# Performance work log

Hardware: AMD Instinct MI355X
Metric: run time of the kernel (lower is better)

The kernel has to match this reference:

```python
import jax, jax.numpy as jnp
import numpy as np


def setup_inputs() -> dict:
    key = jax.random.key(0)
    ks = jax.random.split(key, 6)
    dim, dt_rank, dim_inner, d_state, channels, batch = 1024, 64, 1024, 128, 64, 8
    rn = lambda k, shape, sc: (jax.random.normal(k, shape, jnp.float32) * sc)
    return {
        "x": rn(ks[0], (batch, channels, dim), 1.0),
        "proj_w": rn(ks[1], (dim, dim), dim ** -0.5),
        "proj_b": jnp.zeros((dim,), jnp.float32),
        "conv_w": rn(ks[2], (channels, channels, 3), (channels * 3) ** -0.5),
        "conv_b": jnp.zeros((channels,), jnp.float32),
        "deltaBC_w": rn(ks[3], (dt_rank + 2 * d_state, dim), dim ** -0.5),
        "dt_proj_w": rn(ks[4], (dim_inner, dt_rank), dt_rank ** -0.5),
        "dt_proj_b": jnp.zeros((dim_inner,), jnp.float32),
        "A_log": jnp.log(jnp.broadcast_to(
            jnp.arange(1, d_state + 1, dtype=jnp.float32), (dim_inner, d_state))),
        "D": jnp.ones((dim_inner,), jnp.float32),
    }


def _silu(x):
    return x * jax.nn.sigmoid(x)


def _selective_scan(x, delta, A, B, C, D):
    # x, delta: (b, l, ed); A: (ed, n); B, C: (b, l, n); D: (ed)
    deltaA = jnp.exp(delta[..., None] * A)                      # (b, l, ed, n)
    BX = delta[..., None] * B[:, :, None, :] * x[..., None]     # (b, l, ed, n)

    def binop(e1, e2):
        a1, b1 = e1
        a2, b2 = e2
        return a1 * a2, a2 * b1 + b2

    # h_t = deltaA_t * h_{t-1} + BX_t  (parallel scan over sequence axis)
    _, hs = jax.lax.associative_scan(binop, (deltaA, BX), axis=1)
    y = jnp.einsum("blen,bln->ble", hs, C) + D * x
    return y


def reference(x, proj_w, proj_b, conv_w, conv_b, deltaBC_w,
              dt_proj_w, dt_proj_b, A_log, D):
    dt_rank = dt_proj_w.shape[1]
    d_state = A_log.shape[1]

    skip = x
    # same self.proj applied to both branches
    x1 = x @ proj_w.T + proj_b
    x2 = x1

    # Conv1d over the feature axis, treating seq positions as channels (L == channels)
    x1 = jax.lax.conv_general_dilated(
        x1, conv_w, window_strides=(1,), padding=[(1, 1)],
        dimension_numbers=("NCH", "OIH", "NCH")) + conv_b[None, :, None]
    x1 = _silu(x1)

    # SSM
    A = -jnp.exp(A_log)
    dbc = x1 @ deltaBC_w.T                                      # (b, l, dt_rank + 2n)
    delta = dbc[..., :dt_rank]
    Bm = dbc[..., dt_rank:dt_rank + d_state]
    Cm = dbc[..., dt_rank + d_state:]
    delta = jax.nn.softplus(delta @ dt_proj_w.T + dt_proj_b)    # (b, l, ed)
    y = _selective_scan(x1, delta, A, Bm, Cm, D)

    out = y * _silu(x2) + skip
    return out @ proj_w.T + proj_b
```

## Files before the change

kernel.cpp:

```cpp
#include <hip/hip_runtime.h>
#include <hip/hip_bf16.h>
#include <math.h>

typedef __hip_bfloat16 bf16;
typedef __attribute__((ext_vector_type(8))) short bf16x8;
typedef __attribute__((ext_vector_type(4))) float f32x4;

#define DIM     1024
#define DT_RANK 64
#define D_STATE 128
#define CHAN    64
#define BATCH   8
#define ROWS    (BATCH*CHAN)
#define DBC_N   (DT_RANK + 2*D_STATE)

#define SZ_X    (ROWS*DIM)
#define SZ_PW   (DIM*DIM)
#define SZ_PB   (DIM)
#define SZ_CW   (CHAN*CHAN*3)
#define SZ_CB   (CHAN)
#define SZ_DBCW (DBC_N*DIM)
#define SZ_DTW  (DIM*DT_RANK)
#define SZ_DTB  (DIM)
#define SZ_ALOG (DIM*D_STATE)
#define SZ_D    (DIM)

#define O0 0
#define O1 (O0+SZ_X)
#define O2 (O1+SZ_PW)
#define O3 (O2+SZ_PB)
#define O4 (O3+SZ_CW)
#define O5 (O4+SZ_CB)
#define O6 (O5+SZ_DBCW)
#define O7 (O6+SZ_DTW)
#define O8 (O7+SZ_DTB)
#define O9 (O8+SZ_ALOG)
#define TOTAL (O9+SZ_D)

#define BF16_ONES_PAIR 0x3F803F80u

__device__ __forceinline__ unsigned short f2b(float v) {
    bf16 t = __float2bfloat16(v);
    return *reinterpret_cast<unsigned short*>(&t);
}
__device__ __forceinline__ float b162f(unsigned short s) {
    return __uint_as_float(((unsigned)s) << 16);
}
__device__ __forceinline__ const bf16* SELP(const void* din, const bf16* wsp, int isb) {
    return isb ? (const bf16*)din : wsp;
}

__global__ __launch_bounds__(256) void convert_kernel(
    const void* __restrict__ s0, const void* __restrict__ s1,
    const void* __restrict__ s2, const void* __restrict__ s3,
    const void* __restrict__ s4, const void* __restrict__ s5,
    const void* __restrict__ s6, const void* __restrict__ s7,
    const void* __restrict__ s8, const void* __restrict__ s9,
    bf16* __restrict__ dstb)
{
    if (*(const unsigned*)s9 == BF16_ONES_PAIR) return;
    int idx = (blockIdx.x * 256 + threadIdx.x) * 4;
    if (idx >= TOTAL) return;
    const void* src; int base;
    if      (idx < O1) { src = s0; base = O0; }
    else if (idx < O2) { src = s1; base = O1; }
    else if (idx < O3) { src = s2; base = O2; }
    else if (idx < O4) { src = s3; base = O3; }
    else if (idx < O5) { src = s4; base = O4; }
    else if (idx < O6) { src = s5; base = O5; }
    else if (idx < O7) { src = s6; base = O6; }
    else if (idx < O8) { src = s7; base = O7; }
    else if (idx < O9) { src = s8; base = O8; }
    else               { src = s9; base = O9; }
    const int rel = idx - base;
    float4 v = *reinterpret_cast<const float4*>((const float*)src + rel);
    ushort4 u; u.x = f2b(v.x); u.y = f2b(v.y); u.z = f2b(v.z); u.w = f2b(v.w);
    *reinterpret_cast<ushort4*>(&dstb[idx]) = u;
}

template<int ACT, int OUTMODE, int K>
__global__ __launch_bounds__(256) void gemm_mfma(
    const void* __restrict__ Ad, const bf16* __restrict__ Aw,
    const void* __restrict__ Bd, const bf16* __restrict__ Bw,
    const void* __restrict__ biasd, const bf16* __restrict__ biasw,
    void* __restrict__ C0, bf16* __restrict__ C1,
    int lda, int ldb, int ldc, const unsigned* __restrict__ dsrc)
{
    __shared__ float red[4][32][36];
    const int isb = (*dsrc == BF16_ONES_PAIR) ? 1 : 0;
    const bf16* A = SELP(Ad, Aw, isb);
    const bf16* B = SELP(Bd, Bw, isb);
    const bf16* biasp = (biasd || biasw) ? SELP(biasd, biasw, isb) : nullptr;

    const int l  = threadIdx.x & 63;
    const int w  = threadIdx.x >> 6;
    const int m0 = blockIdx.y * 32;
    const int n0 = blockIdx.x * 32;
    const int fr = l & 15;
    const int ko = (l >> 4) * 8;

    const bf16* Abase = A + (size_t)(m0 + fr) * lda + ko;
    const bf16* Bbase = B + (size_t)(n0 + fr) * ldb + ko;

    f32x4 acc00 = {}, acc01 = {}, acc10 = {}, acc11 = {};

    #pragma unroll 4
    for (int ks = w; ks * 32 < K; ks += 4) {
        const int k0 = ks * 32;
        bf16x8 a0 = *reinterpret_cast<const bf16x8*>(Abase + k0);
        bf16x8 a1 = *reinterpret_cast<const bf16x8*>(Abase + (size_t)16 * lda + k0);
        bf16x8 b0 = *reinterpret_cast<const bf16x8*>(Bbase + k0);
        bf16x8 b1 = *reinterpret_cast<const bf16x8*>(Bbase + (size_t)16 * ldb + k0);
        acc00 = __builtin_amdgcn_mfma_f32_16x16x32_bf16(a0, b0, acc00, 0, 0, 0);
        acc01 = __builtin_amdgcn_mfma_f32_16x16x32_bf16(a0, b1, acc01, 0, 0, 0);
        acc10 = __builtin_amdgcn_mfma_f32_16x16x32_bf16(a1, b0, acc10, 0, 0, 0);
        acc11 = __builtin_amdgcn_mfma_f32_16x16x32_bf16(a1, b1, acc11, 0, 0, 0);
    }

    {
        const int cr = (l >> 4) * 4;
        const int cc = l & 15;
        #pragma unroll
        for (int v = 0; v < 4; ++v) {
            red[w][cr + v][cc]           = acc00[v];
            red[w][cr + v][16 + cc]      = acc01[v];
            red[w][16 + cr + v][cc]      = acc10[v];
            red[w][16 + cr + v][16 + cc] = acc11[v];
        }
    }
    __syncthreads();

    const int t = threadIdx.x;
    const int r = t >> 3;
    const int c = (t & 7) * 4;
    float o[4];
    #pragma unroll
    for (int q = 0; q < 4; ++q) {
        float s = red[0][r][c + q] + red[1][r][c + q]
                + red[2][r][c + q] + red[3][r][c + q];
        if (biasp) s += __bfloat162float(biasp[n0 + c + q]);
        if (ACT == 1) s = (s > 20.0f) ? s : log1pf(__expf(s));
        o[q] = s;
    }
    const int m = m0 + r, nn = n0 + c;
    const size_t off = (size_t)m * ldc + nn;
    if (OUTMODE == 0) {
        *reinterpret_cast<float4*>((float*)C0 + off) = make_float4(o[0], o[1], o[2], o[3]);
    } else if (OUTMODE == 3) {
        ushort4 u; u.x = f2b(o[0]); u.y = f2b(o[1]); u.z = f2b(o[2]); u.w = f2b(o[3]);
        *reinterpret_cast<ushort4*>(C1 + off) = u;
    } else {
        if (isb) {
            ushort4 u; u.x = f2b(o[0]); u.y = f2b(o[1]); u.z = f2b(o[2]); u.w = f2b(o[3]);
            *reinterpret_cast<ushort4*>((bf16*)C0 + off) = u;
        } else {
            *reinterpret_cast<float4*>((float*)C0 + off) = make_float4(o[0], o[1], o[2], o[3]);
        }
    }
}

__global__ __launch_bounds__(256) void conv_silu_kernel(
    const float* __restrict__ xin,
    const void* __restrict__ cwd, const bf16* __restrict__ cww,
    const void* __restrict__ cbd, const bf16* __restrict__ cbw,
    float* __restrict__ xout, bf16* __restrict__ xout_bf,
    const unsigned* __restrict__ dsrc)
{
    const int isb = (*dsrc == BF16_ONES_PAIR) ? 1 : 0;
    const bf16* cw = SELP(cwd, cww, isb);
    const bf16* cb = SELP(cbd, cbw, isb);
    const int n   = blockIdx.x & 7;
    const int o   = blockIdx.x >> 3;
    const int tid = threadIdx.x;
    const int h0  = tid * 4;
    const float* xrow = xin + (size_t)n * CHAN * DIM;
    const bf16* wrow = cw + o * CHAN * 3;
    float acc0 = 0.f, acc1 = 0.f, acc2 = 0.f, acc3 = 0.f;
    #pragma unroll 4
    for (int i = 0; i < CHAN; ++i) {
        const float* xr = xrow + (size_t)i * DIM;
        const float4 xv = *reinterpret_cast<const float4*>(&xr[h0]);
        const float left  = (h0 > 0)        ? xr[h0 - 1] : 0.0f;
        const float right = (h0 + 4 < DIM)  ? xr[h0 + 4] : 0.0f;
        const float w0 = __bfloat162float(wrow[i * 3 + 0]);
        const float w1 = __bfloat162float(wrow[i * 3 + 1]);
        const float w2 = __bfloat162float(wrow[i * 3 + 2]);
        acc0 = fmaf(left, w0, fmaf(xv.x, w1, fmaf(xv.y, w2, acc0)));
        acc1 = fmaf(xv.x, w0, fmaf(xv.y, w1, fmaf(xv.z, w2, acc1)));
        acc2 = fmaf(xv.y, w0, fmaf(xv.z, w1, fmaf(xv.w, w2, acc2)));
        acc3 = fmaf(xv.z, w0, fmaf(xv.w, w1, fmaf(right, w2, acc3)));
    }
    const float bb = __bfloat162float(cb[o]);
    size_t base = (size_t)(n * CHAN + o) * DIM + h0;
    float v0 = acc0 + bb, v1 = acc1 + bb, v2 = acc2 + bb, v3 = acc3 + bb;
    v0 = v0 / (1.0f + __expf(-v0));
    v1 = v1 / (1.0f + __expf(-v1));
    v2 = v2 / (1.0f + __expf(-v2));
    v3 = v3 / (1.0f + __expf(-v3));
    *reinterpret_cast<float4*>(&xout[base]) = make_float4(v0, v1, v2, v3);
    ushort4 u; u.x = f2b(v0); u.y = f2b(v1); u.z = f2b(v2); u.w = f2b(v3);
    *reinterpret_cast<ushort4*>(&xout_bf[base]) = u;
}

__device__ __forceinline__ float sum8_dpp(float x) {
    int v;
    v = __builtin_amdgcn_update_dpp(0, __float_as_int(x), 0x111, 0xf, 0xf, true); x += __int_as_float(v);
    v = __builtin_amdgcn_update_dpp(0, __float_as_int(x), 0x112, 0xf, 0xf, true); x += __int_as_float(v);
    v = __builtin_amdgcn_update_dpp(0, __float_as_int(x), 0x114, 0xf, 0xf, true); x += __int_as_float(v);
    return x;
}

__global__ __launch_bounds__(512) void scan_kernel(
    const void* __restrict__ xd,  const bf16* __restrict__ xw,
    const float* __restrict__ x2,
    const float* __restrict__ xc,
    const bf16*  __restrict__ dbc_bf,
    const void* __restrict__ dtwd, const bf16* __restrict__ dtww,
    const void* __restrict__ dtbd, const bf16* __restrict__ dtbw,
    const void* __restrict__ alogd, const bf16* __restrict__ alogw,
    const void* __restrict__ dvd,  const bf16* __restrict__ dvw,
    bf16*        __restrict__ outp)
{
    __shared__ unsigned short sBC[CHAN][264];
    __shared__ float2 sPart[CHAN][8][8];
    __shared__ float sDB[CHAN][16][2];
    __shared__ float sPxc[CHAN][16];
    const int isb = (*(const unsigned*)dvd == BF16_ONES_PAIR) ? 1 : 0;
    const bf16* x_bf = SELP(xd, xw, isb);
    const bf16* dtw  = SELP(dtwd, dtww, isb);
    const bf16* dtb  = SELP(dtbd, dtbw, isb);
    const bf16* alog = SELP(alogd, alogw, isb);
    const bf16* dvec = SELP(dvd, dvw, isb);

    const int tid  = threadIdx.x;
    const int w    = tid >> 6;
    const int lane = tid & 63;
    const int bb   = blockIdx.x & 7;
    const int eb0  = (blockIdx.x >> 3) * 16;
    const int r0   = bb * CHAN;

    const int e0 = eb0 + 2 * w;
    const float C_LOG2E = 1.44269504f;
    const ushort2 alu0 = *reinterpret_cast<const ushort2*>(
        (const unsigned short*)alog + (size_t)e0 * D_STATE + 2 * lane);
    const ushort2 alu1 = *reinterpret_cast<const ushort2*>(
        (const unsigned short*)alog + (size_t)(e0 + 1) * D_STATE + 2 * lane);
    const float a00 = -__expf(b162f(alu0.x)) * C_LOG2E;
    const float a01 = -__expf(b162f(alu0.y)) * C_LOG2E;
    const float a10 = -__expf(b162f(alu1.x)) * C_LOG2E;
    const float a11 = -__expf(b162f(alu1.y)) * C_LOG2E;

    f32x4 acc = {};
    if (w < 4) {
        const int fr = lane & 15;
        const int ko = (lane >> 4) * 8;
        const bf16* Ab = dbc_bf + (size_t)(r0 + 16 * w + fr) * DBC_N + ko;
        const bf16* Bb = dtw + (size_t)(eb0 + fr) * DT_RANK + ko;
        bf16x8 fa0 = *reinterpret_cast<const bf16x8*>(Ab);
        bf16x8 fa1 = *reinterpret_cast<const bf16x8*>(Ab + 32);
        bf16x8 fb0 = *reinterpret_cast<const bf16x8*>(Bb);
        bf16x8 fb1 = *reinterpret_cast<const bf16x8*>(Bb + 32);
        acc = __builtin_amdgcn_mfma_f32_16x16x32_bf16(fa0, fb0, acc, 0, 0, 0);
        acc = __builtin_amdgcn_mfma_f32_16x16x32_bf16(fa1, fb1, acc, 0, 0, 0);
    } else {
        const int t2 = tid - 256;
        {
            const int row = t2 >> 2, q = t2 & 3;
            const uint4* src = reinterpret_cast<const uint4*>(
                dbc_bf + (size_t)(r0 + row) * DBC_N + DT_RANK + q * 64);
            uint4* dst = reinterpret_cast<uint4*>(&sBC[row][q * 64]);
            #pragma unroll
            for (int k = 0; k < 8; ++k) dst[k] = src[k];
        }
        {
            const int row = t2 >> 2, j = (t2 & 3) * 4;
            const float4 pc = *reinterpret_cast<const float4*>(
                &xc[(size_t)(r0 + row) * DIM + eb0 + j]);
            *reinterpret_cast<float4*>(&sPxc[row][j]) = pc;
        }
    }
    __syncthreads();

    if (w < 4) {
        const int cr = (lane >> 4) * 4, cc = lane & 15;
        const float bia = __bfloat162float(dtb[eb0 + cc]);
        #pragma unroll
        for (int v = 0; v < 4; ++v) {
            const int row = 16 * w + cr + v;
            float pre = acc[v] + bia;
            float dlt = (pre > 20.0f) ? pre : log1pf(__expf(pre));
            sDB[row][cc][0] = dlt;
            sDB[row][cc][1] = dlt * sPxc[row][cc];
        }
    }
    __syncthreads();

    float h00 = 0.f, h01 = 0.f, h10 = 0.f, h11 = 0.f;
    unsigned bu = *reinterpret_cast<const unsigned*>(&sBC[0][2 * lane]);
    unsigned cu = *reinterpret_cast<const unsigned*>(&sBC[0][128 + 2 * lane]);
    float4 db = *reinterpret_cast<const float4*>(&sDB[0][2 * w][0]);

    #pragma unroll 8
    for (int l = 0; l < CHAN; ++l) {
        const int ln = (l + 1) & 63;
        const unsigned bun = *reinterpret_cast<const unsigned*>(&sBC[ln][2 * lane]);
        const unsigned cun = *reinterpret_cast<const unsigned*>(&sBC[ln][128 + 2 * lane]);
        const float4 dbn = *reinterpret_cast<const float4*>(&sDB[ln][2 * w][0]);

        const float bv0 = __uint_as_float(bu << 16);
        const float bv1 = __uint_as_float(bu & 0xffff0000u);
        const float cv0 = __uint_as_float(cu << 16);
        const float cv1 = __uint_as_float(cu & 0xffff0000u);

        const float e00 = __builtin_amdgcn_exp2f(db.x * a00);
        const float e01 = __builtin_amdgcn_exp2f(db.x * a01);
        h00 = fmaf(e00, h00, db.y * bv0);
        h01 = fmaf(e01, h01, db.y * bv1);
        const float p0 = sum8_dpp(fmaf(h00, cv0, h01 * cv1));

        const float e10 = __builtin_amdgcn_exp2f(db.z * a10);
        const float e11 = __builtin_amdgcn_exp2f(db.z * a11);
        h10 = fmaf(e10, h10, db.w * bv0);
        h11 = fmaf(e11, h11, db.w * bv1);
        const float p1 = sum8_dpp(fmaf(h10, cv0, h11 * cv1));

        if ((lane & 7) == 7)
            sPart[l][lane >> 3][w] = make_float2(p0, p1);

        bu = bun; cu = cun; db = dbn;
    }
    __syncthreads();

    {
        const int le = tid >> 3;
        const int wp = tid & 7;
        float y0 = 0.f, y1 = 0.f;
        #pragma unroll
        for (int q = 0; q < 8; ++q) {
            const float2 p = sPart[le][q][wp];
            y0 += p.x; y1 += p.y;
        }
        const int e = eb0 + 2 * wp;
        const size_t off = (size_t)(r0 + le) * DIM + e;
        const float  xv0 = sPxc[le][2 * wp], xv1 = sPxc[le][2 * wp + 1];
        const float2 x2v = *reinterpret_cast<const float2*>(&x2[off]);
        const ushort2 xs = *reinterpret_cast<const ushort2*>(
            (const unsigned short*)x_bf + off);
        const ushort2 dv = *reinterpret_cast<const ushort2*>(
            (const unsigned short*)dvec + e);
        const float ga0 = x2v.x / (1.0f + __expf(-x2v.x));
        const float ga1 = x2v.y / (1.0f + __expf(-x2v.y));
        ushort2 u;
        u.x = f2b(fmaf(y0 + b162f(dv.x) * xv0, ga0, b162f(xs.x)));
        u.y = f2b(fmaf(y1 + b162f(dv.y) * xv1, ga1, b162f(xs.y)));
        *reinterpret_cast<ushort2*>(&outp[off]) = u;
    }
}

extern "C" void kernel_launch(void* const* d_in, const int* in_sizes, int n_in,
                              void* d_out, int out_size, void* d_ws, size_t ws_size,
                              hipStream_t stream) {
    bf16* inB = (bf16*)d_ws;
    float* x1_pre  = (float*)(inB + TOTAL);
    float* x1c     = x1_pre + (size_t)ROWS * DIM;
    bf16*  x1c_bf  = (bf16*)(x1c + (size_t)ROWS * DIM);
    bf16*  dbc_bf  = x1c_bf + (size_t)ROWS * DIM;
    bf16*  outp_bf = dbc_bf + (size_t)ROWS * DBC_N;
    const unsigned* dsrc = (const unsigned*)d_in[9];

    convert_kernel<<<(TOTAL / 4 + 255) / 256, 256, 0, stream>>>(
        d_in[0], d_in[1], d_in[2], d_in[3], d_in[4],
        d_in[5], d_in[6], d_in[7], d_in[8], d_in[9], inB);

    gemm_mfma<0, 0, DIM><<<dim3(DIM / 32, ROWS / 32), 256, 0, stream>>>(
        d_in[0], inB + O0, d_in[1], inB + O1, d_in[2], inB + O2,
        x1_pre, nullptr, DIM, DIM, DIM, dsrc);
    conv_silu_kernel<<<dim3(CHAN * BATCH), 256, 0, stream>>>(
        x1_pre, d_in[3], inB + O3, d_in[4], inB + O4, x1c, x1c_bf, dsrc);
    gemm_mfma<0, 3, DIM><<<dim3(DBC_N / 32, ROWS / 32), 256, 0, stream>>>(
        nullptr, x1c_bf, d_in[5], inB + O5, nullptr, nullptr,
        nullptr, dbc_bf, DIM, DIM, DBC_N, dsrc);
    scan_kernel<<<dim3(BATCH * (DIM / 16)), 512, 0, stream>>>(
        d_in[0], inB + O0, x1_pre, x1c, dbc_bf,
        d_in[6], inB + O6, d_in[7], inB + O7, d_in[8], inB + O8,
        d_in[9], inB + O9, outp_bf);
    gemm_mfma<0, 1, DIM><<<dim3(DIM / 32, ROWS / 32), 256, 0, stream>>>(
        nullptr, outp_bf, d_in[1], inB + O1, d_in[2], inB + O2,
        d_out, nullptr, DIM, DIM, DIM, dsrc);
}
```

Baseline: 89.40 us.

## Fuse input projection GEMM with conv+SiLU and store intermediates in bf16

Replaces the separate projection GEMM and conv_silu kernels with one kernel. Each block computes a 64-row by 32-column tile of the projection plus a 16-column halo on each side, keeps it in shared memory, and applies the feature-axis conv and SiLU there. The fp32 intermediates x1_pre and x1c become bf16 buffers read by the scan kernel, which removes a kernel launch and cuts global memory traffic. In exchange, the GEMM loads operands straight from global memory without LDS tiling, recomputes the halo columns (about 2x the MFMA work), and stores x2 and the conv output at lower precision.

```diff
diff --git a/kernel.cpp b/kernel.cpp
--- a/kernel.cpp
+++ b/kernel.cpp
@@ -78,6 +78,101 @@
     *reinterpret_cast<ushort4*>(&dstb[idx]) = u;
 }
 
+__global__ __launch_bounds__(512) void fused_proj_conv(
+    const void* __restrict__ xd,  const bf16* __restrict__ xw,
+    const void* __restrict__ pwd, const bf16* __restrict__ pww,
+    const void* __restrict__ pbd, const bf16* __restrict__ pbw,
+    const void* __restrict__ cwd, const bf16* __restrict__ cww,
+    const void* __restrict__ cbd, const bf16* __restrict__ cbw,
+    bf16* __restrict__ x2_bf, bf16* __restrict__ x1c_bf,
+    const unsigned* __restrict__ dsrc)
+{
+    __shared__ float sX1[CHAN][68];
+    const int isb = (*dsrc == BF16_ONES_PAIR) ? 1 : 0;
+    const bf16* X  = SELP(xd, xw, isb);
+    const bf16* PW = SELP(pwd, pww, isb);
+    const bf16* PB = SELP(pbd, pbw, isb);
+    const bf16* CW = SELP(cwd, cww, isb);
+    const bf16* CB = SELP(cbd, cbw, isb);
+
+    const int tid  = threadIdx.x;
+    const int w    = tid >> 6;
+    const int lane = tid & 63;
+    const int bb   = blockIdx.x & 7;
+    const int ec   = (blockIdx.x >> 3) * 32;
+    const int r0   = bb * CHAN;
+
+    const int rh = w >> 2;
+    const int ct = w & 3;
+    const int c0 = ec - 16 + ct * 16;
+    const bool valid = (c0 >= 0) && (c0 < DIM);
+
+    if (valid) {
+        const int fr = lane & 15;
+        const int ko = (lane >> 4) * 8;
+        const bf16* Abase = X  + (size_t)(r0 + rh * 32 + fr) * DIM + ko;
+        const bf16* Bbase = PW + (size_t)(c0 + fr) * DIM + ko;
+        f32x4 acc0 = {}, acc1 = {};
+        #pragma unroll 4
+        for (int k0 = 0; k0 < DIM; k0 += 32) {
+            bf16x8 a0 = *reinterpret_cast<const bf16x8*>(Abase + k0);
+            bf16x8 a1 = *reinterpret_cast<const bf16x8*>(Abase + (size_t)16 * DIM + k0);
+            bf16x8 b  = *reinterpret_cast<const bf16x8*>(Bbase + k0);
+            acc0 = __builtin_amdgcn_mfma_f32_16x16x32_bf16(a0, b, acc0, 0, 0, 0);
+            acc1 = __builtin_amdgcn_mfma_f32_16x16x32_bf16(a1, b, acc1, 0, 0, 0);
+        }
+        const int cr = (lane >> 4) * 4;
+        const int cc = lane & 15;
+        const float bias = __bfloat162float(PB[c0 + cc]);
+        #pragma unroll
+        for (int v = 0; v < 4; ++v) {
+            sX1[rh * 32 + cr + v][ct * 16 + cc]      = acc0[v] + bias;
+            sX1[rh * 32 + 16 + cr + v][ct * 16 + cc] = acc1[v] + bias;
+        }
+    } else {
+        const int row = rh * 32 + (lane & 31);
+        const int cb0 = ct * 16 + (lane >> 5) * 8;
+        #pragma unroll
+        for (int j = 0; j < 8; ++j) sX1[row][cb0 + j] = 0.0f;
+    }
+    __syncthreads();
+
+    {
+        const int o  = tid >> 3;
+        const int hq = (tid & 7) * 4;
+        const bf16* wrow = CW + o * (CHAN * 3);
+        float a0 = 0.f, a1 = 0.f, a2 = 0.f, a3 = 0.f;
+        #pragma unroll 4
+        for (int i = 0; i < CHAN; ++i) {
+            const float* win = &sX1[i][16 + hq - 1];
+            const float r0f = win[0], r1f = win[1], r2f = win[2];
+            const float r3f = win[3], r4f = win[4], r5f = win[5];
+            const float w0 = __bfloat162float(wrow[i * 3 + 0]);
+            const float w1 = __bfloat162float(wrow[i * 3 + 1]);
+            const float w2 = __bfloat162float(wrow[i * 3 + 2]);
+            a0 = fmaf(r0f, w0, fmaf(r1f, w1, fmaf(r2f, w2, a0)));
+            a1 = fmaf(r1f, w0, fmaf(r2f, w1, fmaf(r3f, w2, a1)));
+            a2 = fmaf(r2f, w0, fmaf(r3f, w1, fmaf(r4f, w2, a2)));
+            a3 = fmaf(r3f, w0, fmaf(r4f, w1, fmaf(r5f, w2, a3)));
+        }
+        const float bcv = __bfloat162float(CB[o]);
+        float v0 = a0 + bcv, v1 = a1 + bcv, v2 = a2 + bcv, v3 = a3 + bcv;
+        v0 = v0 / (1.0f + __expf(-v0));
+        v1 = v1 / (1.0f + __expf(-v1));
+        v2 = v2 / (1.0f + __expf(-v2));
+        v3 = v3 / (1.0f + __expf(-v3));
+        const size_t base = (size_t)(r0 + o) * DIM + ec + hq;
+        ushort4 uc; uc.x = f2b(v0); uc.y = f2b(v1); uc.z = f2b(v2); uc.w = f2b(v3);
+        *reinterpret_cast<ushort4*>(&x1c_bf[base]) = uc;
+        ushort4 u2;
+        u2.x = f2b(sX1[o][16 + hq + 0]);
+        u2.y = f2b(sX1[o][16 + hq + 1]);
+        u2.z = f2b(sX1[o][16 + hq + 2]);
+        u2.w = f2b(sX1[o][16 + hq + 3]);
+        *reinterpret_cast<ushort4*>(&x2_bf[base]) = u2;
+    }
+}
+
 template<int ACT, int OUTMODE, int K>
 __global__ __launch_bounds__(256) void gemm_mfma(
     const void* __restrict__ Ad, const bf16* __restrict__ Aw,
@@ -159,49 +254,6 @@
     }
 }
 
-__global__ __launch_bounds__(256) void conv_silu_kernel(
-    const float* __restrict__ xin,
-    const void* __restrict__ cwd, const bf16* __restrict__ cww,
-    const void* __restrict__ cbd, const bf16* __restrict__ cbw,
-    float* __restrict__ xout, bf16* __restrict__ xout_bf,
-    const unsigned* __restrict__ dsrc)
-{
-    const int isb = (*dsrc == BF16_ONES_PAIR) ? 1 : 0;
-    const bf16* cw = SELP(cwd, cww, isb);
-    const bf16* cb = SELP(cbd, cbw, isb);
-    const int n   = blockIdx.x & 7;
-    const int o   = blockIdx.x >> 3;
-    const int tid = threadIdx.x;
-    const int h0  = tid * 4;
-    const float* xrow = xin + (size_t)n * CHAN * DIM;
-    const bf16* wrow = cw + o * CHAN * 3;
-    float acc0 = 0.f, acc1 = 0.f, acc2 = 0.f, acc3 = 0.f;
-    #pragma unroll 4
-    for (int i = 0; i < CHAN; ++i) {
-        const float* xr = xrow + (size_t)i * DIM;
-        const float4 xv = *reinterpret_cast<const float4*>(&xr[h0]);
-        const float left  = (h0 > 0)        ? xr[h0 - 1] : 0.0f;
-        const float right = (h0 + 4 < DIM)  ? xr[h0 + 4] : 0.0f;
-        const float w0 = __bfloat162float(wrow[i * 3 + 0]);
-        const float w1 = __bfloat162float(wrow[i * 3 + 1]);
-        const float w2 = __bfloat162float(wrow[i * 3 + 2]);
-        acc0 = fmaf(left, w0, fmaf(xv.x, w1, fmaf(xv.y, w2, acc0)));
-        acc1 = fmaf(xv.x, w0, fmaf(xv.y, w1, fmaf(xv.z, w2, acc1)));
-        acc2 = fmaf(xv.y, w0, fmaf(xv.z, w1, fmaf(xv.w, w2, acc2)));
-        acc3 = fmaf(xv.z, w0, fmaf(xv.w, w1, fmaf(right, w2, acc3)));
-    }
-    const float bb = __bfloat162float(cb[o]);
-    size_t base = (size_t)(n * CHAN + o) * DIM + h0;
-    float v0 = acc0 + bb, v1 = acc1 + bb, v2 = acc2 + bb, v3 = acc3 + bb;
-    v0 = v0 / (1.0f + __expf(-v0));
-    v1 = v1 / (1.0f + __expf(-v1));
-    v2 = v2 / (1.0f + __expf(-v2));
-    v3 = v3 / (1.0f + __expf(-v3));
-    *reinterpret_cast<float4*>(&xout[base]) = make_float4(v0, v1, v2, v3);
-    ushort4 u; u.x = f2b(v0); u.y = f2b(v1); u.z = f2b(v2); u.w = f2b(v3);
-    *reinterpret_cast<ushort4*>(&xout_bf[base]) = u;
-}
-
 __device__ __forceinline__ float sum8_dpp(float x) {
     int v;
     v = __builtin_amdgcn_update_dpp(0, __float_as_int(x), 0x111, 0xf, 0xf, true); x += __int_as_float(v);
@@ -212,8 +264,8 @@
 
 __global__ __launch_bounds__(512) void scan_kernel(
     const void* __restrict__ xd,  const bf16* __restrict__ xw,
-    const float* __restrict__ x2,
-    const float* __restrict__ xc,
+    const bf16*  __restrict__ x2bf,
+    const bf16*  __restrict__ xcbf,
     const bf16*  __restrict__ dbc_bf,
     const void* __restrict__ dtwd, const bf16* __restrict__ dtww,
     const void* __restrict__ dtbd, const bf16* __restrict__ dtbw,
@@ -274,9 +326,12 @@
         }
         {
             const int row = t2 >> 2, j = (t2 & 3) * 4;
-            const float4 pc = *reinterpret_cast<const float4*>(
-                &xc[(size_t)(r0 + row) * DIM + eb0 + j]);
-            *reinterpret_cast<float4*>(&sPxc[row][j]) = pc;
+            const ushort4 pc = *reinterpret_cast<const ushort4*>(
+                (const unsigned short*)xcbf + (size_t)(r0 + row) * DIM + eb0 + j);
+            sPxc[row][j + 0] = b162f(pc.x);
+            sPxc[row][j + 1] = b162f(pc.y);
+            sPxc[row][j + 2] = b162f(pc.z);
+            sPxc[row][j + 3] = b162f(pc.w);
         }
     }
     __syncthreads();
@@ -343,13 +398,15 @@
         const int e = eb0 + 2 * wp;
         const size_t off = (size_t)(r0 + le) * DIM + e;
         const float  xv0 = sPxc[le][2 * wp], xv1 = sPxc[le][2 * wp + 1];
-        const float2 x2v = *reinterpret_cast<const float2*>(&x2[off]);
+        const ushort2 x2u = *reinterpret_cast<const ushort2*>(
+            (const unsigned short*)x2bf + off);
         const ushort2 xs = *reinterpret_cast<const ushort2*>(
             (const unsigned short*)x_bf + off);
         const ushort2 dv = *reinterpret_cast<const ushort2*>(
             (const unsigned short*)dvec + e);
-        const float ga0 = x2v.x / (1.0f + __expf(-x2v.x));
-        const float ga1 = x2v.y / (1.0f + __expf(-x2v.y));
+        const float x20 = b162f(x2u.x), x21 = b162f(x2u.y);
+        const float ga0 = x20 / (1.0f + __expf(-x20));
+        const float ga1 = x21 / (1.0f + __expf(-x21));
         ushort2 u;
         u.x = f2b(fmaf(y0 + b162f(dv.x) * xv0, ga0, b162f(xs.x)));
         u.y = f2b(fmaf(y1 + b162f(dv.y) * xv1, ga1, b162f(xs.y)));
@@ -361,29 +418,29 @@
                               void* d_out, int out_size, void* d_ws, size_t ws_size,
                               hipStream_t stream) {
     bf16* inB = (bf16*)d_ws;
-    float* x1_pre  = (float*)(inB + TOTAL);
-    float* x1c     = x1_pre + (size_t)ROWS * DIM;
-    bf16*  x1c_bf  = (bf16*)(x1c + (size_t)ROWS * DIM);
-    bf16*  dbc_bf  = x1c_bf + (size_t)ROWS * DIM;
-    bf16*  outp_bf = dbc_bf + (size_t)ROWS * DBC_N;
+    bf16* x2_bf   = inB + TOTAL;
+    bf16* x1c_bf  = x2_bf + (size_t)ROWS * DIM;
+    bf16* dbc_bf  = x1c_bf + (size_t)ROWS * DIM;
+    bf16* outp_bf = dbc_bf + (size_t)ROWS * DBC_N;
     const unsigned* dsrc = (const unsigned*)d_in[9];
 
     convert_kernel<<<(TOTAL / 4 + 255) / 256, 256, 0, stream>>>(
         d_in[0], d_in[1], d_in[2], d_in[3], d_in[4],
         d_in[5], d_in[6], d_in[7], d_in[8], d_in[9], inB);
 
-    gemm_mfma<0, 0, DIM><<<dim3(DIM / 32, ROWS / 32), 256, 0, stream>>>(
+    fused_proj_conv<<<dim3(BATCH * (DIM / 32)), 512, 0, stream>>>(
         d_in[0], inB + O0, d_in[1], inB + O1, d_in[2], inB + O2,
-        x1_pre, nullptr, DIM, DIM, DIM, dsrc);
-    conv_silu_kernel<<<dim3(CHAN * BATCH), 256, 0, stream>>>(
-        x1_pre, d_in[3], inB + O3, d_in[4], inB + O4, x1c, x1c_bf, dsrc);
+        d_in[3], inB + O3, d_in[4], inB + O4, x2_bf, x1c_bf, dsrc);
+
     gemm_mfma<0, 3, DIM><<<dim3(DBC_N / 32, ROWS / 32), 256, 0, stream>>>(
         nullptr, x1c_bf, d_in[5], inB + O5, nullptr, nullptr,
         nullptr, dbc_bf, DIM, DIM, DBC_N, dsrc);
+
     scan_kernel<<<dim3(BATCH * (DIM / 16)), 512, 0, stream>>>(
-        d_in[0], inB + O0, x1_pre, x1c, dbc_bf,
+        d_in[0], inB + O0, x2_bf, x1c_bf, dbc_bf,
         d_in[6], inB + O6, d_in[7], inB + O7, d_in[8], inB + O8,
         d_in[9], inB + O9, outp_bf);
+
     gemm_mfma<0, 1, DIM><<<dim3(DIM / 32, ROWS / 32), 256, 0, stream>>>(
         nullptr, outp_bf, d_in[1], inB + O1, d_in[2], inB + O2,
         d_out, nullptr, DIM, DIM, DIM, dsrc);
```

Measured after the change: 78.31 us. -12.4%, faster.
